# Optimization experiments

Hardware: AMD Instinct MI355X
Metric: run time of the kernel (lower is better)

Reference implementation:

```python
import jax, jax.numpy as jnp
import numpy as np

T, B, I, H = 512, 256, 512, 512


def setup_inputs() -> dict:
    key = jax.random.key(0)
    ks = jax.random.split(key, 10)
    inp = {
        "x": jax.random.normal(ks[0], (T, B, I), dtype=jnp.float32),
        "lengths": jax.random.randint(ks[1], (B,), 1, T + 1).astype(jnp.int64),
        # LSTMCell params, gate order [i, f, g, o]; forget-gate bias init to 1
        "W_ih": jax.random.normal(ks[2], (4 * H, I), dtype=jnp.float32) / np.sqrt(I),
        "W_hh": jax.random.normal(ks[3], (4 * H, H), dtype=jnp.float32) / np.sqrt(H),
        "b_ih": jnp.zeros((4 * H,), jnp.float32).at[H:2 * H].set(1.0),
        "b_hh": jnp.zeros((4 * H,), jnp.float32),
        # multiplicative projections
        "mx_w": jax.random.normal(ks[4], (H, I), dtype=jnp.float32) / np.sqrt(I),
        "mx_b": jnp.zeros((H,), jnp.float32),
        "mh_w": jax.random.normal(ks[5], (H, H), dtype=jnp.float32) / np.sqrt(H),
        "mh_b": jnp.zeros((H,), jnp.float32),
        "h0": jnp.zeros((H,), jnp.float32),
        "c0": jnp.zeros((H,), jnp.float32),
    }
    return inp


def _mlstm(x, lengths, W_ih, W_hh, b_ih, b_hh, mx_w, mx_b, mh_w, mh_b, h0, c0):
    Tn, Bn, _ = x.shape
    Hn = h0.shape[0]
    # Precompute all input-side projections in two big GEMMs (batched over T*B).
    xg = jnp.einsum('tbi,gi->tbg', x, W_ih) + b_ih          # [T,B,4H]
    xm = jnp.einsum('tbi,hi->tbh', x, mx_w) + mx_b          # [T,B,H]
    # active[t,b] = t < lengths[b]; padded steps freeze (h,c) -> packed semantics
    active = (jnp.arange(Tn)[:, None] < lengths[None, :])[..., None]  # [T,B,1]

    def step(carry, inp):
        h, c = carry
        xg_t, xm_t, act = inp
        m = xm_t * (h @ mh_w.T + mh_b)                       # multiplicative hidden
        gates = xg_t + m @ W_hh.T + b_hh                     # cell(x, (m, c))
        i, f, g, o = jnp.split(gates, 4, axis=-1)
        c_new = jax.nn.sigmoid(f) * c + jax.nn.sigmoid(i) * jnp.tanh(g)
        h_new = jax.nn.sigmoid(o) * jnp.tanh(c_new)
        h = jnp.where(act, h_new, h)
        c = jnp.where(act, c_new, c)
        return (h, c), None

    h_init = jnp.broadcast_to(h0, (Bn, Hn))
    c_init = jnp.broadcast_to(c0, (Bn, Hn))
    (h, c), _ = jax.lax.scan(step, (h_init, c_init), (xg, xm, active))
    # Torch code returns final cell state of each sequence, in batch order.
    return c


def reference(x, lengths, W_ih, W_hh, b_ih, b_hh, mx_w, mx_b, mh_w, mh_b, h0, c0):
    return _mlstm(x, lengths, W_ih, W_hh, b_ih, b_hh, mx_w, mx_b, mh_w, mh_b, h0, c0)
```

## Files before the change

kernel.cpp:

```cpp
#include <hip/hip_runtime.h>
#include <stdint.h>


typedef __attribute__((ext_vector_type(8))) short s8v;
typedef __attribute__((ext_vector_type(8))) _Float16 h8v;
typedef __attribute__((ext_vector_type(4))) float f4v;

#define SC 2048.0f
#define ISC (1.0f / 2048.0f)

__device__ __forceinline__ f4v mf(s8v a, s8v b, f4v c) {
  return __builtin_amdgcn_mfma_f32_16x16x32_f16(
      __builtin_bit_cast(h8v, a), __builtin_bit_cast(h8v, b), c, 0, 0, 0);
}
__device__ __forceinline__ uint16_t f2h(float x) {
  _Float16 h = (_Float16)x;
  return __builtin_bit_cast(uint16_t, h);
}
__device__ __forceinline__ void split2(float v, uint16_t& hi, uint16_t& lo) {
  _Float16 h = (_Float16)v;
  float r = v - (float)h;
  hi = __builtin_bit_cast(uint16_t, h);
  lo = f2h(r * SC);
}
__device__ __forceinline__ float sigm(float x) { return 1.0f / (1.0f + __expf(-x)); }
__device__ __forceinline__ float tanh_f(float x) { return 1.0f - 2.0f / (__expf(2.0f * x) + 1.0f); }

__device__ __forceinline__ s8v ldx4_sc1(const uint16_t* p) {
  s8v r;
  asm volatile("global_load_dwordx4 %0, %1, off sc1" : "=v"(r) : "v"(p));
  return r;
}
__device__ __forceinline__ uint32_t ld32_sc1(const uint32_t* p) {
  uint32_t r;
  asm volatile("global_load_dword %0, %1, off sc1" : "=v"(r) : "v"(p));
  return r;
}
__device__ __forceinline__ void st16_sc1(uint16_t* p, uint32_t v) {
  asm volatile("global_store_short %0, %1, off sc1" ::"v"(p), "v"(v) : "memory");
}
__device__ __forceinline__ void st32_sc1(uint32_t* p, uint32_t v) {
  asm volatile("global_store_dword %0, %1, off sc1" ::"v"(p), "v"(v) : "memory");
}
#define VM0                                              \
  do {                                                   \
    asm volatile("s_waitcnt vmcnt(0)" ::: "memory");     \
    __builtin_amdgcn_sched_barrier(0);                   \
  } while (0)

__global__ __launch_bounds__(256) void k_split(const float* __restrict__ x,
                                               uint16_t* __restrict__ xh,
                                               uint16_t* __restrict__ xl, long n) {
  long i = ((long)blockIdx.x * 256 + threadIdx.x) * 8;
  if (i >= n) return;
  float4 a = *(const float4*)(x + i);
  float4 b = *(const float4*)(x + i + 4);
  union { uint16_t u[8]; s8v v; } oh, ol;
  float vv[8] = {a.x, a.y, a.z, a.w, b.x, b.y, b.z, b.w};
#pragma unroll
  for (int k = 0; k < 8; ++k) split2(vv[k], oh.u[k], ol.u[k]);
  *(s8v*)(xh + i) = oh.v;
  *(s8v*)(xl + i) = ol.v;
}

__global__ __launch_bounds__(64) void k_packw(const float* __restrict__ Wg,
                                              const float* __restrict__ Wm,
                                              uint16_t* __restrict__ wh,
                                              uint16_t* __restrict__ wl) {
  int s = blockIdx.x >> 4, kt = blockIdx.x & 15, l = threadIdx.x;
  const float* src = (s < 128) ? (Wg + (size_t)(s * 16 + (l & 15)) * 512)
                               : (Wm + (size_t)((s - 128) * 16 + (l & 15)) * 512);
  int k0 = kt * 32 + (l >> 4) * 8;
  float4 a = *(const float4*)(src + k0);
  float4 b = *(const float4*)(src + k0 + 4);
  union { uint16_t u[8]; s8v v; } oh, ol;
  float vv[8] = {a.x, a.y, a.z, a.w, b.x, b.y, b.z, b.w};
#pragma unroll
  for (int k = 0; k < 8; ++k) split2(vv[k], oh.u[k], ol.u[k]);
  size_t adr = ((size_t)(s * 16 + kt) * 64 + l) * 8;
  *(s8v*)(wh + adr) = oh.v;
  *(s8v*)(wl + adr) = ol.v;
}

__device__ __forceinline__ void gpass(const uint16_t* __restrict__ Ap,
                                      const uint16_t* __restrict__ Bp,
                                      s8v* Asm, s8v* Bsm, int rowbase, int s0,
                                      f4v (&acc)[4][4]) {
  int tid = threadIdx.x;
  int wv = tid >> 6, l = tid & 63, wm = wv >> 1, wn = wv & 1;
  int arow = tid >> 1, ahalf = tid & 1, swz = (arow & 7) << 4;
  for (int ks = 0; ks < 8; ++ks) {
    __syncthreads();
    const uint16_t* asrc = Ap + (size_t)(rowbase + arow) * 512 + ks * 64;
#pragma unroll
    for (int q = 0; q < 4; ++q) {
      int pb = ahalf * 64 + q * 16;
      Asm[arow * 8 + (pb >> 4)] = *(const s8v*)(asrc + ((pb ^ swz) >> 1));
    }
#pragma unroll
    for (int q = 0; q < 4; ++q) {
      int ofs = tid * 64 + q * 16;
      int si = ofs >> 11, kti = (ofs >> 10) & 1, inner = ofs & 1023;
      Bsm[ofs >> 4] =
          *(const s8v*)(Bp + (size_t)((s0 + si) * 16 + ks * 2 + kti) * 512 + (inner >> 1));
    }
    __syncthreads();
#pragma unroll
    for (int kti = 0; kti < 2; ++kti) {
      s8v a[4], b[4];
#pragma unroll
      for (int i = 0; i < 4; ++i) {
        int row = wm * 64 + i * 16 + (l & 15);
        int lb = kti * 64 + (l >> 4) * 16;
        a[i] = Asm[row * 8 + ((lb ^ ((l & 7) << 4)) >> 4)];
      }
#pragma unroll
      for (int jj = 0; jj < 4; ++jj) b[jj] = Bsm[((wn * 4 + jj) * 2 + kti) * 64 + l];
#pragma unroll
      for (int i = 0; i < 4; ++i)
#pragma unroll
        for (int jj = 0; jj < 4; ++jj) acc[i][jj] = mf(a[i], b[jj], acc[i][jj]);
    }
  }
}

__global__ __launch_bounds__(256, 2) void k_gemm3(const uint16_t* __restrict__ xh,
                                                  const uint16_t* __restrict__ xl,
                                                  const uint16_t* __restrict__ wh,
                                                  const uint16_t* __restrict__ wl,
                                                  float* __restrict__ blob, int row0) {
  __shared__ s8v Asm[1024], Bsm[1024];
  f4v acc_a[4][4], acc_c[4][4];
#pragma unroll
  for (int i = 0; i < 4; ++i)
#pragma unroll
    for (int jj = 0; jj < 4; ++jj) {
      acc_a[i][jj] = (f4v){0.f, 0.f, 0.f, 0.f};
      acc_c[i][jj] = (f4v){0.f, 0.f, 0.f, 0.f};
    }
  int s0 = blockIdx.x * 8, r0 = blockIdx.y * 128;
  int rowbase = row0 + r0;
  gpass(xh, wh, Asm, Bsm, rowbase, s0, acc_a);
  gpass(xh, wl, Asm, Bsm, rowbase, s0, acc_c);
  gpass(xl, wh, Asm, Bsm, rowbase, s0, acc_c);
  int tid = threadIdx.x, wv = tid >> 6, l = tid & 63, wm = wv >> 1, wn = wv & 1;
#pragma unroll
  for (int i = 0; i < 4; ++i)
#pragma unroll
    for (int jj = 0; jj < 4; ++jj) {
      int s = s0 + wn * 4 + jj;
#pragma unroll
      for (int ri = 0; ri < 4; ++ri) {
        int trow = r0 + wm * 64 + i * 16 + (l >> 4) * 4 + ri;
        int tt = trow >> 8, gg = (trow >> 4) & 15, rr = trow & 15;
        size_t adr = ((size_t)(tt * 160 + s) * 16 + gg) * 256 + rr * 16 + (l & 15);
        blob[adr] = acc_a[i][jj][ri] + acc_c[i][jj][ri] * ISC;
      }
    }
}

__device__ __forceinline__ void spoll(const uint32_t* slots, uint32_t ep, int l) {
  const uint32_t* q = slots + (l & 31);
  for (;;) {
    uint32_t v = ld32_sc1(q);
    VM0;
    if (__all((int)(v >= ep))) break;
    __builtin_amdgcn_s_sleep(1);
  }
}

__global__ __launch_bounds__(128, 1) void k_rec(
    const uint16_t* __restrict__ wrh, const uint16_t* __restrict__ wrl,
    const float* __restrict__ blob,
    const float* __restrict__ b_ih, const float* __restrict__ b_hh,
    const float* __restrict__ mx_b, const float* __restrict__ mh_b,
    const float* __restrict__ h0, const float* __restrict__ c0,
    const int* __restrict__ lengths,
    uint16_t* hh, uint16_t* hl, uint16_t* mhp, uint16_t* mlp,
    float* cbuf, uint32_t* flags, float* out, int chunk) {
  extern __shared__ char smraw[];
  s8v* SW = (s8v*)smraw;
  int tid = threadIdx.x, l = tid & 63, wv = tid >> 6;
  int j = blockIdx.x >> 3, gg = ((blockIdx.x & 7) << 1) | wv;

#pragma unroll
  for (int sl = 0; sl < 9; ++sl) {
    int gs = (sl < 4) ? (sl * 32 + j) : (sl < 8 ? (sl - 4) * 32 + j : 128 + j);
    const s8v* src = (const s8v*)(((sl < 4) ? wrh : wrl) + (size_t)gs * 8192);
#pragma unroll
    for (int it = 0; it < 8; ++it) SW[sl * 1024 + it * 128 + tid] = src[it * 128 + tid];
  }
  s8v wmh[16];
  {
    const s8v* sH = (const s8v*)(wrh + (size_t)(128 + j) * 8192);
#pragma unroll
    for (int kt = 0; kt < 16; ++kt) wmh[kt] = sH[kt * 64 + l];
  }
  __syncthreads();

  int cidx = l & 15, rq = l >> 4;
  int hc = j * 16 + cidx;
  float mhb = mh_b[hc], mxb = mx_b[hc];
  float bsum[4];
#pragma unroll
  for (int nt = 0; nt < 4; ++nt) bsum[nt] = b_ih[nt * 512 + hc] + b_hh[nt * 512 + hc];
  int rowA = gg * 16 + cidx;
  int kofs = rq * 8;
  int rowC0 = gg * 16 + rq * 4;
  float creg[4];
  int lenr[4];
#pragma unroll
  for (int ri = 0; ri < 4; ++ri) {
    int r = rowC0 + ri;
    lenr[ri] = lengths[r];
    creg[ri] = (chunk == 0) ? c0[hc] : cbuf[(size_t)r * 512 + hc];
  }
  uint32_t* mslot = flags + gg * 32;
  uint32_t* hslot = flags + 512 + gg * 32;

  if (chunk == 0) {
    uint16_t hi, lo;
    split2(h0[hc], hi, lo);
#pragma unroll
    for (int ri = 0; ri < 4; ++ri) {
      st16_sc1(hh + (size_t)(rowC0 + ri) * 512 + hc, hi);
      st16_sc1(hl + (size_t)(rowC0 + ri) * 512 + hc, lo);
    }
  }
  asm volatile("s_waitcnt vmcnt(0)" ::: "memory");
  if (l == 0) st32_sc1(hslot + j, 1u);
  spoll(hslot, 1u, l);

  const uint16_t* hrb = hh + (size_t)rowA * 512 + kofs;
  const uint16_t* lrb = hl + (size_t)rowA * 512 + kofs;
  const uint16_t* mrb = mhp + (size_t)rowA * 512 + kofs;
  const uint16_t* nrb = mlp + (size_t)rowA * 512 + kofs;

  for (int t = 0; t < 128; ++t) {
    size_t tb = ((size_t)(t * 160) * 16 + (size_t)gg) * 256 + rq * 64 + cidx;
    float bxm[4], bg[4][4];
#pragma unroll
    for (int ri = 0; ri < 4; ++ri) {
      bxm[ri] = blob[tb + (size_t)(128 + j) * 4096 + ri * 16];
#pragma unroll
      for (int nt = 0; nt < 4; ++nt)
        bg[nt][ri] = blob[tb + (size_t)(nt * 32 + j) * 4096 + ri * 16];
    }
    if (t > 0) spoll(hslot, (uint32_t)(t + 1), l);
    s8v af[16];
#pragma unroll
    for (int kt = 0; kt < 16; ++kt) af[kt] = ldx4_sc1(hrb + kt * 32);
    VM0;
    f4v a1a0 = (f4v){0,0,0,0}, a1a1 = (f4v){0,0,0,0};
    f4v a1c0 = (f4v){0,0,0,0}, a1c1 = (f4v){0,0,0,0};
#pragma unroll
    for (int kt = 0; kt < 16; kt += 2) {
      a1a0 = mf(af[kt], wmh[kt], a1a0);
      a1a1 = mf(af[kt + 1], wmh[kt + 1], a1a1);
    }
#pragma unroll
    for (int kt = 0; kt < 16; ++kt) a1c0 = mf(af[kt], SW[8 * 1024 + kt * 64 + l], a1c0);
#pragma unroll
    for (int kt = 0; kt < 16; ++kt) af[kt] = ldx4_sc1(lrb + kt * 32);
    VM0;
#pragma unroll
    for (int kt = 0; kt < 16; ++kt) a1c1 = mf(af[kt], wmh[kt], a1c1);
#pragma unroll
    for (int ri = 0; ri < 4; ++ri) {
      float hv = a1a0[ri] + a1a1[ri] + (a1c0[ri] + a1c1[ri]) * ISC + mhb;
      float mv = (bxm[ri] + mxb) * hv;
      uint16_t hi, lo;
      split2(mv, hi, lo);
      st16_sc1(mhp + (size_t)(rowC0 + ri) * 512 + hc, hi);
      st16_sc1(mlp + (size_t)(rowC0 + ri) * 512 + hc, lo);
    }
    asm volatile("s_waitcnt vmcnt(0)" ::: "memory");
    if (l == 0) st32_sc1(mslot + j, (uint32_t)(t + 1));
    spoll(mslot, (uint32_t)(t + 1), l);
    f4v p2a[4], p2c[4], p2d[4];
#pragma unroll
    for (int nt = 0; nt < 4; ++nt) {
      p2a[nt] = (f4v){0,0,0,0};
      p2c[nt] = (f4v){0,0,0,0};
      p2d[nt] = (f4v){0,0,0,0};
    }
#pragma unroll
    for (int kt = 0; kt < 16; ++kt) af[kt] = ldx4_sc1(mrb + kt * 32);
    VM0;
#pragma unroll
    for (int kt = 0; kt < 16; ++kt)
#pragma unroll
      for (int nt = 0; nt < 4; ++nt) {
        p2a[nt] = mf(af[kt], SW[nt * 1024 + kt * 64 + l], p2a[nt]);
        p2c[nt] = mf(af[kt], SW[(4 + nt) * 1024 + kt * 64 + l], p2c[nt]);
      }
#pragma unroll
    for (int kt = 0; kt < 16; ++kt) af[kt] = ldx4_sc1(nrb + kt * 32);
    VM0;
#pragma unroll
    for (int kt = 0; kt < 16; ++kt)
#pragma unroll
      for (int nt = 0; nt < 4; ++nt) p2d[nt] = mf(af[kt], SW[nt * 1024 + kt * 64 + l], p2d[nt]);
#pragma unroll
    for (int ri = 0; ri < 4; ++ri) {
      float gi = p2a[0][ri] + (p2c[0][ri] + p2d[0][ri]) * ISC + bsum[0] + bg[0][ri];
      float gf = p2a[1][ri] + (p2c[1][ri] + p2d[1][ri]) * ISC + bsum[1] + bg[1][ri];
      float gc = p2a[2][ri] + (p2c[2][ri] + p2d[2][ri]) * ISC + bsum[2] + bg[2][ri];
      float go = p2a[3][ri] + (p2c[3][ri] + p2d[3][ri]) * ISC + bsum[3] + bg[3][ri];
      float iv = sigm(gi), fv = sigm(gf), gv = tanh_f(gc), ov = sigm(go);
      float cn = fv * creg[ri] + iv * gv;
      float hn = ov * tanh_f(cn);
      bool act = (chunk * 128 + t) < lenr[ri];
      if (act) {
        creg[ri] = cn;
        uint16_t hi, lo;
        split2(hn, hi, lo);
        st16_sc1(hh + (size_t)(rowC0 + ri) * 512 + hc, hi);
        st16_sc1(hl + (size_t)(rowC0 + ri) * 512 + hc, lo);
      }
    }
    if (t < 127) {
      asm volatile("s_waitcnt vmcnt(0)" ::: "memory");
      if (l == 0) st32_sc1(hslot + j, (uint32_t)(t + 2));
    }
  }
#pragma unroll
  for (int ri = 0; ri < 4; ++ri) {
    cbuf[(size_t)(rowC0 + ri) * 512 + hc] = creg[ri];
    if (chunk == 3) out[(size_t)(rowC0 + ri) * 512 + hc] = creg[ri];
  }
}

extern "C" void kernel_launch(void* const* d_in, const int* in_sizes, int n_in,
                              void* d_out, int out_size, void* d_ws, size_t ws_size,
                              hipStream_t stream) {
  (void)in_sizes; (void)n_in; (void)out_size;
  const float* x = (const float*)d_in[0];
  const int* lengths = (const int*)d_in[1];
  const float* W_ih = (const float*)d_in[2];
  const float* W_hh = (const float*)d_in[3];
  const float* b_ih = (const float*)d_in[4];
  const float* b_hh = (const float*)d_in[5];
  const float* mx_w = (const float*)d_in[6];
  const float* mx_b = (const float*)d_in[7];
  const float* mh_w = (const float*)d_in[8];
  const float* mh_b = (const float*)d_in[9];
  const float* h0 = (const float*)d_in[10];
  const float* c0 = (const float*)d_in[11];

  if (ws_size < 616042496ull) return;

  char* ws = (char*)d_ws;
  uint16_t* xh = (uint16_t*)(ws);
  uint16_t* xl = (uint16_t*)(ws + 134217728ull);
  uint16_t* wpre_h = (uint16_t*)(ws + 268435456ull);
  uint16_t* wpre_l = (uint16_t*)(ws + 271056896ull);
  uint16_t* wrec_h = (uint16_t*)(ws + 273678336ull);
  uint16_t* wrec_l = (uint16_t*)(ws + 276299776ull);
  float* blob = (float*)(ws + 278921216ull);
  uint16_t* hh = (uint16_t*)(ws + 614465536ull);
  uint16_t* hl = (uint16_t*)(ws + 614727680ull);
  uint16_t* mhp = (uint16_t*)(ws + 614989824ull);
  uint16_t* mlp = (uint16_t*)(ws + 615251968ull);
  float* cbuf = (float*)(ws + 615514112ull);
  uint32_t* flags = (uint32_t*)(ws + 616038400ull);

  k_split<<<32768, 256, 0, stream>>>(x, xh, xl, 67108864L);
  k_packw<<<2560, 64, 0, stream>>>(W_ih, mx_w, wpre_h, wpre_l);
  k_packw<<<2560, 64, 0, stream>>>(W_hh, mh_w, wrec_h, wrec_l);
  hipFuncSetAttribute(reinterpret_cast<const void*>(k_rec),
                      hipFuncAttributeMaxDynamicSharedMemorySize, 147456);
  for (int c = 0; c < 4; ++c) {
    k_gemm3<<<dim3(20, 256), 256, 0, stream>>>(xh, xl, wpre_h, wpre_l, blob, c * 32768);
    hipMemsetAsync(flags, 0, 4096, stream);
    k_rec<<<256, 128, 147456, stream>>>(wrec_h, wrec_l, blob, b_ih, b_hh, mx_b, mh_b,
                                        h0, c0, lengths, hh, hl, mhp, mlp, cbuf,
                                        flags, (float*)d_out, c);
  }
}
```

Baseline: 8.448 ms.

## Replace flag-based step barriers with parity bits packed into h/m data words

Stops signalling recurrent steps through separate flag slots and polls. Each h and m value is now stored as one 32-bit word holding the fp16 hi and lo parts, with the lowest bit of lo carrying the parity of the timestep. Consumers poll the data words directly until every parity bit matches, then unpack and feed the MFMAs, which removes the separate flag store/wait round trips and the memset. This drops one mantissa bit of the lo part and relies on single-dword stores being seen atomically; every row's h is rewritten each step, even inactive ones, to keep parity current.

```diff
diff --git a/kernel.cpp b/kernel.cpp
--- a/kernel.cpp
+++ b/kernel.cpp
@@ -5,6 +5,7 @@
 typedef __attribute__((ext_vector_type(8))) short s8v;
 typedef __attribute__((ext_vector_type(8))) _Float16 h8v;
 typedef __attribute__((ext_vector_type(4))) float f4v;
+typedef __attribute__((ext_vector_type(4))) uint32_t u4v;
 
 #define SC 2048.0f
 #define ISC (1.0f / 2048.0f)
@@ -23,30 +24,61 @@
   hi = __builtin_bit_cast(uint16_t, h);
   lo = f2h(r * SC);
 }
+__device__ __forceinline__ float unpk1(uint32_t w) {
+  _Float16 h = __builtin_bit_cast(_Float16, (uint16_t)(w >> 16));
+  _Float16 lo = __builtin_bit_cast(_Float16, (uint16_t)(w & 0xFFFEu));
+  return (float)h + (float)lo * ISC;
+}
 __device__ __forceinline__ float sigm(float x) { return 1.0f / (1.0f + __expf(-x)); }
 __device__ __forceinline__ float tanh_f(float x) { return 1.0f - 2.0f / (__expf(2.0f * x) + 1.0f); }
 
-__device__ __forceinline__ s8v ldx4_sc1(const uint16_t* p) {
-  s8v r;
+__device__ __forceinline__ u4v ldp(const uint32_t* p) {
+  u4v r;
   asm volatile("global_load_dwordx4 %0, %1, off sc1" : "=v"(r) : "v"(p));
   return r;
 }
-__device__ __forceinline__ uint32_t ld32_sc1(const uint32_t* p) {
-  uint32_t r;
-  asm volatile("global_load_dword %0, %1, off sc1" : "=v"(r) : "v"(p));
-  return r;
-}
-__device__ __forceinline__ void st16_sc1(uint16_t* p, uint32_t v) {
-  asm volatile("global_store_short %0, %1, off sc1" ::"v"(p), "v"(v) : "memory");
-}
-__device__ __forceinline__ void st32_sc1(uint32_t* p, uint32_t v) {
-  asm volatile("global_store_dword %0, %1, off sc1" ::"v"(p), "v"(v) : "memory");
-}
-#define VM0                                              \
-  do {                                                   \
-    asm volatile("s_waitcnt vmcnt(0)" ::: "memory");     \
-    __builtin_amdgcn_sched_barrier(0);                   \
+__device__ __forceinline__ void st_pk(uint32_t* p, float v, uint32_t par) {
+  uint16_t hi, lo;
+  split2(v, hi, lo);
+  uint32_t w = ((uint32_t)lo & 0xFFFEu) | par | ((uint32_t)hi << 16);
+  asm volatile("global_store_dword %0, %1, off sc1" ::"v"(p), "v"(w) : "memory");
+}
+#define VM0                                          \
+  do {                                               \
+    asm volatile("s_waitcnt vmcnt(0)" ::: "memory"); \
+    __builtin_amdgcn_sched_barrier(0);               \
   } while (0)
+
+#define POLLB(BASE, KT0, PAR)                                              \
+  for (;;) {                                                               \
+    _Pragma("unroll")                                                      \
+    for (int q = 0; q < 8; ++q) {                                          \
+      pk[2 * q] = ldp((BASE) + ((KT0) + q) * 32);                          \
+      pk[2 * q + 1] = ldp((BASE) + ((KT0) + q) * 32 + 4);                  \
+    }                                                                      \
+    VM0;                                                                   \
+    uint32_t _acc = 0;                                                     \
+    _Pragma("unroll")                                                      \
+    for (int q = 0; q < 16; ++q)                                           \
+      _acc |= (pk[q].x ^ (PAR)) | (pk[q].y ^ (PAR)) |                      \
+              (pk[q].z ^ (PAR)) | (pk[q].w ^ (PAR));                       \
+    if (__all((int)((_acc & 1u) == 0u))) break;                            \
+  }
+
+#define UNPK(A, B, HI, LO)                                                 \
+  {                                                                        \
+    union { uint32_t u[4]; s8v s; } _h, _l;                                \
+    _l.u[0] = ((A).x & 0xFFFFu) | ((A).y << 16);                           \
+    _l.u[1] = ((A).z & 0xFFFFu) | ((A).w << 16);                           \
+    _l.u[2] = ((B).x & 0xFFFFu) | ((B).y << 16);                           \
+    _l.u[3] = ((B).z & 0xFFFFu) | ((B).w << 16);                           \
+    _h.u[0] = ((A).x >> 16) | ((A).y & 0xFFFF0000u);                       \
+    _h.u[1] = ((A).z >> 16) | ((A).w & 0xFFFF0000u);                       \
+    _h.u[2] = ((B).x >> 16) | ((B).y & 0xFFFF0000u);                       \
+    _h.u[3] = ((B).z >> 16) | ((B).w & 0xFFFF0000u);                       \
+    HI = _h.s;                                                             \
+    LO = _l.s;                                                             \
+  }
 
 __global__ __launch_bounds__(256) void k_split(const float* __restrict__ x,
                                                uint16_t* __restrict__ xh,
@@ -82,6 +114,17 @@
   *(s8v*)(wl + adr) = ol.v;
 }
 
+__global__ __launch_bounds__(256) void k_init(const float* __restrict__ h0,
+                                              uint32_t* __restrict__ hpk,
+                                              uint32_t* __restrict__ mpk) {
+  int idx = blockIdx.x * 256 + threadIdx.x;
+  int col = idx & 511;
+  uint16_t hi, lo;
+  split2(h0[col], hi, lo);
+  hpk[idx] = ((uint32_t)lo & 0xFFFEu) | ((uint32_t)hi << 16);
+  mpk[idx] = 1u;
+}
+
 __device__ __forceinline__ void gpass(const uint16_t* __restrict__ Ap,
                                       const uint16_t* __restrict__ Bp,
                                       s8v* Asm, s8v* Bsm, int rowbase, int s0,
@@ -159,29 +202,17 @@
     }
 }
 
-__device__ __forceinline__ void spoll(const uint32_t* slots, uint32_t ep, int l) {
-  const uint32_t* q = slots + (l & 31);
-  for (;;) {
-    uint32_t v = ld32_sc1(q);
-    VM0;
-    if (__all((int)(v >= ep))) break;
-    __builtin_amdgcn_s_sleep(1);
-  }
-}
-
 __global__ __launch_bounds__(128, 1) void k_rec(
     const uint16_t* __restrict__ wrh, const uint16_t* __restrict__ wrl,
     const float* __restrict__ blob,
     const float* __restrict__ b_ih, const float* __restrict__ b_hh,
     const float* __restrict__ mx_b, const float* __restrict__ mh_b,
-    const float* __restrict__ h0, const float* __restrict__ c0,
-    const int* __restrict__ lengths,
-    uint16_t* hh, uint16_t* hl, uint16_t* mhp, uint16_t* mlp,
-    float* cbuf, uint32_t* flags, float* out, int chunk) {
+    const float* __restrict__ c0, const int* __restrict__ lengths,
+    uint32_t* hpk, uint32_t* mpk, float* cbuf, float* out, int chunk) {
   extern __shared__ char smraw[];
   s8v* SW = (s8v*)smraw;
   int tid = threadIdx.x, l = tid & 63, wv = tid >> 6;
-  int j = blockIdx.x >> 3, gg = ((blockIdx.x & 7) << 1) | wv;
+  int bid = blockIdx.x, j = bid >> 3, gg = ((bid & 7) << 1) | wv;
 
 #pragma unroll
   for (int sl = 0; sl < 9; ++sl) {
@@ -207,36 +238,23 @@
   int rowA = gg * 16 + cidx;
   int kofs = rq * 8;
   int rowC0 = gg * 16 + rq * 4;
-  float creg[4];
+  float creg[4], hreg[4];
   int lenr[4];
 #pragma unroll
   for (int ri = 0; ri < 4; ++ri) {
     int r = rowC0 + ri;
     lenr[ri] = lengths[r];
     creg[ri] = (chunk == 0) ? c0[hc] : cbuf[(size_t)r * 512 + hc];
-  }
-  uint32_t* mslot = flags + gg * 32;
-  uint32_t* hslot = flags + 512 + gg * 32;
-
-  if (chunk == 0) {
-    uint16_t hi, lo;
-    split2(h0[hc], hi, lo);
-#pragma unroll
-    for (int ri = 0; ri < 4; ++ri) {
-      st16_sc1(hh + (size_t)(rowC0 + ri) * 512 + hc, hi);
-      st16_sc1(hl + (size_t)(rowC0 + ri) * 512 + hc, lo);
-    }
-  }
-  asm volatile("s_waitcnt vmcnt(0)" ::: "memory");
-  if (l == 0) st32_sc1(hslot + j, 1u);
-  spoll(hslot, 1u, l);
-
-  const uint16_t* hrb = hh + (size_t)rowA * 512 + kofs;
-  const uint16_t* lrb = hl + (size_t)rowA * 512 + kofs;
-  const uint16_t* mrb = mhp + (size_t)rowA * 512 + kofs;
-  const uint16_t* nrb = mlp + (size_t)rowA * 512 + kofs;
+    hreg[ri] = unpk1(hpk[(size_t)r * 512 + hc]);
+  }
+
+  const uint32_t* hrb = hpk + (size_t)rowA * 512 + kofs;
+  const uint32_t* mrb = mpk + (size_t)rowA * 512 + kofs;
 
   for (int t = 0; t < 128; ++t) {
+    int tg = chunk * 128 + t;
+    uint32_t parC = (uint32_t)(tg & 1);
+    uint32_t parN = (uint32_t)((tg + 1) & 1);
     size_t tb = ((size_t)(t * 160) * 16 + (size_t)gg) * 256 + rq * 64 + cidx;
     float bxm[4], bg[4][4];
 #pragma unroll
@@ -246,61 +264,65 @@
       for (int nt = 0; nt < 4; ++nt)
         bg[nt][ri] = blob[tb + (size_t)(nt * 32 + j) * 4096 + ri * 16];
     }
-    if (t > 0) spoll(hslot, (uint32_t)(t + 1), l);
-    s8v af[16];
-#pragma unroll
-    for (int kt = 0; kt < 16; ++kt) af[kt] = ldx4_sc1(hrb + kt * 32);
-    VM0;
-    f4v a1a0 = (f4v){0,0,0,0}, a1a1 = (f4v){0,0,0,0};
-    f4v a1c0 = (f4v){0,0,0,0}, a1c1 = (f4v){0,0,0,0};
-#pragma unroll
-    for (int kt = 0; kt < 16; kt += 2) {
-      a1a0 = mf(af[kt], wmh[kt], a1a0);
-      a1a1 = mf(af[kt + 1], wmh[kt + 1], a1a1);
-    }
-#pragma unroll
-    for (int kt = 0; kt < 16; ++kt) a1c0 = mf(af[kt], SW[8 * 1024 + kt * 64 + l], a1c0);
-#pragma unroll
-    for (int kt = 0; kt < 16; ++kt) af[kt] = ldx4_sc1(lrb + kt * 32);
-    VM0;
-#pragma unroll
-    for (int kt = 0; kt < 16; ++kt) a1c1 = mf(af[kt], wmh[kt], a1c1);
+    u4v pk[16];
+    f4v a1a = (f4v){0, 0, 0, 0}, a1c0 = (f4v){0, 0, 0, 0}, a1c1 = (f4v){0, 0, 0, 0};
+    POLLB(hrb, 0, parC);
+#pragma unroll
+    for (int q = 0; q < 8; ++q) {
+      s8v hi_, lo_;
+      UNPK(pk[2 * q], pk[2 * q + 1], hi_, lo_);
+      a1a = mf(hi_, wmh[q], a1a);
+      a1c0 = mf(hi_, SW[8 * 1024 + q * 64 + l], a1c0);
+      a1c1 = mf(lo_, wmh[q], a1c1);
+    }
+    POLLB(hrb, 8, parC);
+#pragma unroll
+    for (int q = 0; q < 8; ++q) {
+      int kt = 8 + q;
+      s8v hi_, lo_;
+      UNPK(pk[2 * q], pk[2 * q + 1], hi_, lo_);
+      a1a = mf(hi_, wmh[kt], a1a);
+      a1c0 = mf(hi_, SW[8 * 1024 + kt * 64 + l], a1c0);
+      a1c1 = mf(lo_, wmh[kt], a1c1);
+    }
 #pragma unroll
     for (int ri = 0; ri < 4; ++ri) {
-      float hv = a1a0[ri] + a1a1[ri] + (a1c0[ri] + a1c1[ri]) * ISC + mhb;
+      float hv = a1a[ri] + (a1c0[ri] + a1c1[ri]) * ISC + mhb;
       float mv = (bxm[ri] + mxb) * hv;
-      uint16_t hi, lo;
-      split2(mv, hi, lo);
-      st16_sc1(mhp + (size_t)(rowC0 + ri) * 512 + hc, hi);
-      st16_sc1(mlp + (size_t)(rowC0 + ri) * 512 + hc, lo);
-    }
-    asm volatile("s_waitcnt vmcnt(0)" ::: "memory");
-    if (l == 0) st32_sc1(mslot + j, (uint32_t)(t + 1));
-    spoll(mslot, (uint32_t)(t + 1), l);
+      st_pk(mpk + (size_t)(rowC0 + ri) * 512 + hc, mv, parC);
+    }
     f4v p2a[4], p2c[4], p2d[4];
 #pragma unroll
     for (int nt = 0; nt < 4; ++nt) {
-      p2a[nt] = (f4v){0,0,0,0};
-      p2c[nt] = (f4v){0,0,0,0};
-      p2d[nt] = (f4v){0,0,0,0};
-    }
-#pragma unroll
-    for (int kt = 0; kt < 16; ++kt) af[kt] = ldx4_sc1(mrb + kt * 32);
-    VM0;
-#pragma unroll
-    for (int kt = 0; kt < 16; ++kt)
+      p2a[nt] = (f4v){0, 0, 0, 0};
+      p2c[nt] = (f4v){0, 0, 0, 0};
+      p2d[nt] = (f4v){0, 0, 0, 0};
+    }
+    POLLB(mrb, 0, parC);
+#pragma unroll
+    for (int q = 0; q < 8; ++q) {
+      s8v hi_, lo_;
+      UNPK(pk[2 * q], pk[2 * q + 1], hi_, lo_);
 #pragma unroll
       for (int nt = 0; nt < 4; ++nt) {
-        p2a[nt] = mf(af[kt], SW[nt * 1024 + kt * 64 + l], p2a[nt]);
-        p2c[nt] = mf(af[kt], SW[(4 + nt) * 1024 + kt * 64 + l], p2c[nt]);
-      }
-#pragma unroll
-    for (int kt = 0; kt < 16; ++kt) af[kt] = ldx4_sc1(nrb + kt * 32);
-    VM0;
-#pragma unroll
-    for (int kt = 0; kt < 16; ++kt)
-#pragma unroll
-      for (int nt = 0; nt < 4; ++nt) p2d[nt] = mf(af[kt], SW[nt * 1024 + kt * 64 + l], p2d[nt]);
+        p2a[nt] = mf(hi_, SW[nt * 1024 + q * 64 + l], p2a[nt]);
+        p2c[nt] = mf(hi_, SW[(4 + nt) * 1024 + q * 64 + l], p2c[nt]);
+        p2d[nt] = mf(lo_, SW[nt * 1024 + q * 64 + l], p2d[nt]);
+      }
+    }
+    POLLB(mrb, 8, parC);
+#pragma unroll
+    for (int q = 0; q < 8; ++q) {
+      int kt = 8 + q;
+      s8v hi_, lo_;
+      UNPK(pk[2 * q], pk[2 * q + 1], hi_, lo_);
+#pragma unroll
+      for (int nt = 0; nt < 4; ++nt) {
+        p2a[nt] = mf(hi_, SW[nt * 1024 + kt * 64 + l], p2a[nt]);
+        p2c[nt] = mf(hi_, SW[(4 + nt) * 1024 + kt * 64 + l], p2c[nt]);
+        p2d[nt] = mf(lo_, SW[nt * 1024 + kt * 64 + l], p2d[nt]);
+      }
+    }
 #pragma unroll
     for (int ri = 0; ri < 4; ++ri) {
       float gi = p2a[0][ri] + (p2c[0][ri] + p2d[0][ri]) * ISC + bsum[0] + bg[0][ri];
@@ -310,18 +332,12 @@
       float iv = sigm(gi), fv = sigm(gf), gv = tanh_f(gc), ov = sigm(go);
       float cn = fv * creg[ri] + iv * gv;
       float hn = ov * tanh_f(cn);
-      bool act = (chunk * 128 + t) < lenr[ri];
+      bool act = tg < lenr[ri];
       if (act) {
         creg[ri] = cn;
-        uint16_t hi, lo;
-        split2(hn, hi, lo);
-        st16_sc1(hh + (size_t)(rowC0 + ri) * 512 + hc, hi);
-        st16_sc1(hl + (size_t)(rowC0 + ri) * 512 + hc, lo);
-      }
-    }
-    if (t < 127) {
-      asm volatile("s_waitcnt vmcnt(0)" ::: "memory");
-      if (l == 0) st32_sc1(hslot + j, (uint32_t)(t + 2));
+        hreg[ri] = hn;
+      }
+      st_pk(hpk + (size_t)(rowC0 + ri) * 512 + hc, hreg[ri], parN);
     }
   }
 #pragma unroll
@@ -348,7 +364,7 @@
   const float* h0 = (const float*)d_in[10];
   const float* c0 = (const float*)d_in[11];
 
-  if (ws_size < 616042496ull) return;
+  if (ws_size < 616038400ull) return;
 
   char* ws = (char*)d_ws;
   uint16_t* xh = (uint16_t*)(ws);
@@ -358,23 +374,19 @@
   uint16_t* wrec_h = (uint16_t*)(ws + 273678336ull);
   uint16_t* wrec_l = (uint16_t*)(ws + 276299776ull);
   float* blob = (float*)(ws + 278921216ull);
-  uint16_t* hh = (uint16_t*)(ws + 614465536ull);
-  uint16_t* hl = (uint16_t*)(ws + 614727680ull);
-  uint16_t* mhp = (uint16_t*)(ws + 614989824ull);
-  uint16_t* mlp = (uint16_t*)(ws + 615251968ull);
+  uint32_t* hpk = (uint32_t*)(ws + 614465536ull);
+  uint32_t* mpk = (uint32_t*)(ws + 614989824ull);
   float* cbuf = (float*)(ws + 615514112ull);
-  uint32_t* flags = (uint32_t*)(ws + 616038400ull);
 
   k_split<<<32768, 256, 0, stream>>>(x, xh, xl, 67108864L);
   k_packw<<<2560, 64, 0, stream>>>(W_ih, mx_w, wpre_h, wpre_l);
   k_packw<<<2560, 64, 0, stream>>>(W_hh, mh_w, wrec_h, wrec_l);
+  k_init<<<512, 256, 0, stream>>>(h0, hpk, mpk);
   hipFuncSetAttribute(reinterpret_cast<const void*>(k_rec),
                       hipFuncAttributeMaxDynamicSharedMemorySize, 147456);
   for (int c = 0; c < 4; ++c) {
     k_gemm3<<<dim3(20, 256), 256, 0, stream>>>(xh, xl, wpre_h, wpre_l, blob, c * 32768);
-    hipMemsetAsync(flags, 0, 4096, stream);
     k_rec<<<256, 128, 147456, stream>>>(wrec_h, wrec_l, blob, b_ih, b_hh, mx_b, mh_b,
-                                        h0, c0, lengths, hh, hl, mhp, mlp, cbuf,
-                                        flags, (float*)d_out, c);
-  }
-}
+                                        c0, lengths, hpk, mpk, cbuf, (float*)d_out, c);
+  }
+}
```

Measured after the change: 8.586 ms. No clear change (+1.6%).
